# Optimization experiments

Hardware: AMD Instinct MI355X
Metric: run time of the kernel (lower is better)

Reference implementation:

```python
import jax, jax.numpy as jnp
import numpy as np
import math

D_MODEL = 1024
N_HEADS = 16
D_HEAD = 64
D_MLP = 4096
SEQ = 2048
BATCH = 1
BLOCK_INDEX = 2
PREV_NODES = (N_HEADS + 1) * BLOCK_INDEX + 1  # 35
ROTARY_DIM = 64
ROTARY_BASE = 10000
IGNORE = -100000.0
LN_EPS = 1e-5


def setup_inputs() -> dict:
    key = jax.random.key(0)
    ks = jax.random.split(key, 20)
    s = 0.02
    return {
        "resid_pre": jax.random.normal(ks[0], (BATCH, SEQ, PREV_NODES, D_MODEL), jnp.float32),
        "W_Q": s * jax.random.normal(ks[1], (N_HEADS, D_MODEL, D_HEAD), jnp.float32),
        "b_Q": jnp.zeros((N_HEADS, D_HEAD), jnp.float32),
        "W_K": s * jax.random.normal(ks[2], (N_HEADS, D_MODEL, D_HEAD), jnp.float32),
        "b_K": jnp.zeros((N_HEADS, D_HEAD), jnp.float32),
        "W_V": s * jax.random.normal(ks[3], (N_HEADS, D_MODEL, D_HEAD), jnp.float32),
        "b_V": jnp.zeros((N_HEADS, D_HEAD), jnp.float32),
        "W_O": s * jax.random.normal(ks[4], (N_HEADS, D_HEAD, D_MODEL), jnp.float32),
        "b_O": jnp.zeros((D_MODEL,), jnp.float32),
        "mask_q_logits": 0.01 * jax.random.normal(ks[5], (PREV_NODES, N_HEADS), jnp.float32),
        "mask_k_logits": 0.01 * jax.random.normal(ks[6], (PREV_NODES, N_HEADS), jnp.float32),
        "mask_v_logits": 0.01 * jax.random.normal(ks[7], (PREV_NODES, N_HEADS), jnp.float32),
        "mask_mlp_logits": 0.01 * jax.random.normal(ks[8], (PREV_NODES + N_HEADS,), jnp.float32),
        "W_in": s * jax.random.normal(ks[9], (D_MODEL, D_MLP), jnp.float32),
        "b_in": jnp.zeros((D_MLP,), jnp.float32),
        "W_out": s * jax.random.normal(ks[10], (D_MLP, D_MODEL), jnp.float32),
        "b_out": jnp.zeros((D_MODEL,), jnp.float32),
    }


def _rotary_sin_cos(seq_len):
    pos = jnp.arange(seq_len, dtype=jnp.float32)
    dim = jnp.arange(ROTARY_DIM // 2, dtype=jnp.float32)
    freq = ROTARY_BASE ** (dim / (ROTARY_DIM / 2))
    freq = jnp.concatenate([freq, freq])  # '(2 d)' repeat (non-adjacent pairs)
    angles = pos[:, None] / freq[None, :]  # [seq, rotary_dim]
    return jnp.sin(angles), jnp.cos(angles)


def _apply_rotary(x, sin, cos):
    # x: [B, S, H, d_head]; rotary_dim == d_head here
    n = ROTARY_DIM // 2
    x_rot = x[..., :ROTARY_DIM]
    flip = jnp.concatenate([-x_rot[..., n:], x_rot[..., :n]], axis=-1)
    rotated = x_rot * cos[None, :, None, :] + flip * sin[None, :, None, :]
    return jnp.concatenate([rotated, x[..., ROTARY_DIM:]], axis=-1)


def _ln_pre(x):
    # LayerNormPre: center + scale over last dim, no learned params
    x = x - jnp.mean(x, axis=-1, keepdims=True)
    scale = jnp.sqrt(jnp.mean(x * x, axis=-1, keepdims=True) + LN_EPS)
    return x / scale


def reference(resid_pre, W_Q, b_Q, W_K, b_K, W_V, b_V, W_O, b_O,
              mask_q_logits, mask_k_logits, mask_v_logits, mask_mlp_logits,
              W_in, b_in, W_out, b_out):
    B, S = resid_pre.shape[0], resid_pre.shape[1]
    # deterministic edge masks
    m_q = jnp.where(mask_q_logits > 0.0, 1.0, 0.0)
    m_k = jnp.where(mask_k_logits > 0.0, 1.0, 0.0)
    m_v = jnp.where(mask_v_logits > 0.0, 1.0, 0.0)
    m_mlp = jnp.where(mask_mlp_logits > 0.0, 1.0, 0.0)

    # per-head masked residual streams: [B, S, n_heads, d_model]
    res_q = jnp.einsum('bpnm,nh->bphm', resid_pre, m_q)
    res_k = jnp.einsum('bpnm,nh->bphm', resid_pre, m_k)
    res_v = jnp.einsum('bpnm,nh->bphm', resid_pre, m_v)

    nq = _ln_pre(res_q)
    nk = _ln_pre(res_k)
    nv = _ln_pre(res_v)

    # attention (per-head projections)
    q = jnp.einsum('bshm,hmd->bshd', nq, W_Q) + b_Q
    k = jnp.einsum('bshm,hmd->bshd', nk, W_K) + b_K
    sin, cos = _rotary_sin_cos(S)
    q = _apply_rotary(q, sin, cos)
    k = _apply_rotary(k, sin, cos)

    scores = jnp.einsum('bqhd,bkhd->bhqk', q, k) / math.sqrt(D_HEAD)
    causal = jnp.triu(jnp.ones((S, S), dtype=bool), k=1)
    scores = jnp.where(causal[None, None], IGNORE, scores)
    pattern = jax.nn.softmax(scores, axis=-1)

    v = jnp.einsum('bshm,hmd->bshd', nv, W_V) + b_V
    z = jnp.einsum('bhqk,bkhd->bqhd', pattern, v)
    # per-head attn output (heads NOT summed): [B, S, n_heads, d_model]
    attn_out = jnp.einsum('bqhd,hdm->bqhm', z, W_O) + b_O / N_HEADS

    # grow residual stream with attention head nodes
    residual = jnp.concatenate([resid_pre, attn_out], axis=2)  # [B,S,prev+H,dm]

    masked_mlp_residual = jnp.einsum('bpnm,n->bpm', residual, m_mlp)
    norm_mid = _ln_pre(masked_mlp_residual)
    mlp_out = jax.nn.gelu(norm_mid @ W_in + b_in, approximate=True) @ W_out + b_out

    out = jnp.concatenate([residual, mlp_out[:, :, None, :]], axis=2)
    return out
```

## Files before the change

kernel.cpp:

```cpp
#include <hip/hip_runtime.h>
#include <stdint.h>


#define SEQ 2048
#define DM 1024
#define NHEADS 16
#define DH 64
#define DMLP 4096
#define PN 35
#define TOTN 51
#define OUTN 52
#define LNEPS 1e-5f
#define L2E 1.44269504088896340736f

typedef __bf16 bf16x8 __attribute__((ext_vector_type(8)));
typedef float f32x4 __attribute__((ext_vector_type(4)));
typedef unsigned short u16x8 __attribute__((ext_vector_type(8)));

static __device__ __forceinline__ unsigned short f2bf(float f) {
    unsigned int u = __builtin_bit_cast(unsigned int, f);
    u += 0x7fffu + ((u >> 16) & 1u);
    return (unsigned short)(u >> 16);
}

static __device__ __forceinline__ float gelu_tanh(float x) {
    float u = 0.7978845608028654f * x * (1.f + 0.044715f * x * x);
    float e = exp2f(u * (2.f * L2E));
    float th = 1.f - 2.f / (e + 1.f);
    return 0.5f * x * (1.f + th);
}

static __device__ __forceinline__ void gload_lds16(const void* g, void* l) {
    __builtin_amdgcn_global_load_lds(
        (const __attribute__((address_space(1))) unsigned int*)g,
        (__attribute__((address_space(3))) unsigned int*)l, 16, 0, 0);
}

static __device__ __forceinline__ int swz_src(int lane) {
    return ((lane & 7) ^ ((lane >> 3) & 7)) * 8;
}
static __device__ __forceinline__ int swz_off(int r, int g) {
    return ((g ^ (r & 7)) * 16);
}

__global__ void prep_all(const float* __restrict__ mq, const float* __restrict__ mk,
                         const float* __restrict__ mv, const float* __restrict__ mmlp,
                         const float* __restrict__ bQ, const float* __restrict__ bK,
                         const float* __restrict__ bV,
                         float* __restrict__ rot, unsigned long long* __restrict__ maskbits,
                         float* __restrict__ mlpmaskf, float* __restrict__ biasQKV,
                         float* __restrict__ colWqkv, float* __restrict__ colWin) {
    int bid = blockIdx.x, tid = threadIdx.x;
    if (bid < 256) {
        int id = bid * 256 + tid;
        int s = id >> 5, j = id & 31;
        float freq = powf(10000.f, (float)j * (1.f / 32.f));
        float ang = (float)s / freq;
        rot[s * 64 + j] = sinf(ang);
        rot[s * 64 + 32 + j] = cosf(ang);
    } else if (bid == 256) {
        if (tid < 48) {
            int ty = tid >> 4, h = tid & 15;
            const float* src = (ty == 0) ? mq : (ty == 1 ? mk : mv);
            unsigned long long bits = 0;
            for (int n = 0; n < PN; ++n)
                if (src[n * NHEADS + h] > 0.f) bits |= 1ull << n;
            maskbits[tid] = bits;
            const float* bsrc = (ty == 0) ? bQ : (ty == 1 ? bK : bV);
            for (int d = 0; d < DH; ++d) biasQKV[tid * 64 + d] = bsrc[h * DH + d];
        }
        if (tid == 48) {
            unsigned long long bits = 0;
            for (int n = 0; n < PN; ++n)
                if (mmlp[n] > 0.f) bits |= 1ull << n;
            maskbits[48] = bits;
        }
        if (tid < 64) mlpmaskf[tid] = (tid < TOTN && mmlp[tid] > 0.f) ? 1.f : 0.f;
    } else if (bid == 257) {
        for (int i = tid; i < 3072; i += 256) colWqkv[i] = 0.f;
    } else {
        int base = (bid - 258) * 2048;
        for (int i = tid; i < 2048; i += 256) colWin[base + i] = 0.f;
    }
}

__global__ void wtrans(const float* __restrict__ in, unsigned short* __restrict__ out,
                       int K, int N, size_t inZ, size_t outZ,
                       float* __restrict__ colsum, size_t colZ) {
    int z = blockIdx.z;
    const float* ib = in + (size_t)z * inZ;
    unsigned short* ob = out + (size_t)z * outZ;
    __shared__ float t[32][33];
    int n0 = blockIdx.x * 32, k0 = blockIdx.y * 32;
    int tx = threadIdx.x & 31, ty = threadIdx.x >> 5;
#pragma unroll
    for (int r = 0; r < 4; ++r) {
        int k = ty + r * 8;
        t[k][tx] = ib[(size_t)(k0 + k) * N + n0 + tx];
    }
    __syncthreads();
#pragma unroll
    for (int r = 0; r < 4; ++r) {
        int n = ty + r * 8;
        ob[(size_t)(n0 + n) * K + k0 + tx] = f2bf(t[tx][n]);
    }
    if (colsum != nullptr && ty == 0) {
        float s = 0.f;
#pragma unroll
        for (int k = 0; k < 32; ++k) s += t[k][tx];
        atomicAdd(&colsum[(size_t)z * colZ + n0 + tx], s);
    }
}

__launch_bounds__(512, 1)
__global__ void k1_masked_norm(const float* __restrict__ resid,
                               const unsigned long long* __restrict__ maskbits,
                               float* __restrict__ outp,
                               unsigned short* __restrict__ nrm,
                               float* __restrict__ stats,
                               float* __restrict__ prevpart) {
    int s = blockIdx.x;
    int tid = threadIdx.x;
    int lane = tid & 63, w = tid >> 6;
    const float2* rp = (const float2*)(resid + (size_t)s * PN * DM);
    float2* outv = (float2*)(outp + (size_t)s * OUTN * DM);
    float2 r[PN];
#pragma unroll
    for (int n = 0; n < PN; ++n) {
        float2 v = rp[n * (DM / 2) + tid];
        r[n] = v;
        outv[n * (DM / 2) + tid] = v;
    }
    __shared__ float wpart[8][48][2];
#pragma unroll 1
    for (int th = 0; th < 48; ++th) {
        unsigned long long bits = maskbits[th];
        float sx = 0.f, sy = 0.f;
#pragma unroll
        for (int n = 0; n < PN; ++n) {
            if ((bits >> n) & 1ull) { sx += r[n].x; sy += r[n].y; }
        }
        unsigned int pk = (unsigned int)f2bf(sx) | ((unsigned int)f2bf(sy) << 16);
        ((unsigned int*)nrm)[((size_t)th * SEQ + s) * (DM / 2) + tid] = pk;
        float p1 = sx + sy, p2 = sx * sx + sy * sy;
#pragma unroll
        for (int d = 1; d < 64; d <<= 1) {
            p1 += __shfl_xor(p1, d);
            p2 += __shfl_xor(p2, d);
        }
        if (lane == 0) { wpart[w][th][0] = p1; wpart[w][th][1] = p2; }
    }
    {
        unsigned long long bits = maskbits[48];
        float px = 0.f, py = 0.f;
#pragma unroll
        for (int n = 0; n < PN; ++n) {
            if ((bits >> n) & 1ull) { px += r[n].x; py += r[n].y; }
        }
        ((float2*)prevpart)[(size_t)s * (DM / 2) + tid] = make_float2(px, py);
    }
    __syncthreads();
    if (tid < 48) {
        float S1 = 0.f, S2 = 0.f;
        for (int ww = 0; ww < 8; ++ww) { S1 += wpart[ww][tid][0]; S2 += wpart[ww][tid][1]; }
        float mean = S1 * (1.f / DM);
        float var = S2 * (1.f / DM) - mean * mean;
        float* st = stats + ((size_t)tid * SEQ + s) * 2;
        st[0] = mean;
        st[1] = rsqrtf(var + LNEPS);
    }
}

__launch_bounds__(256, 4)
__global__ void stats_k(const float* __restrict__ midf, float* __restrict__ stats) {
    int s = blockIdx.x, tid = threadIdx.x;
    int lane = tid & 63, w = tid >> 6;
    float4 v = ((const float4*)midf)[(size_t)s * (DM / 4) + tid];
    float p1 = v.x + v.y + v.z + v.w;
    float p2 = v.x * v.x + v.y * v.y + v.z * v.z + v.w * v.w;
#pragma unroll
    for (int d = 1; d < 64; d <<= 1) { p1 += __shfl_xor(p1, d); p2 += __shfl_xor(p2, d); }
    __shared__ float wp[4][2];
    if (lane == 0) { wp[w][0] = p1; wp[w][1] = p2; }
    __syncthreads();
    if (tid == 0) {
        float S1 = wp[0][0] + wp[1][0] + wp[2][0] + wp[3][0];
        float S2 = wp[0][1] + wp[1][1] + wp[2][1] + wp[3][1];
        float mean = S1 * (1.f / DM);
        float var = S2 * (1.f / DM) - mean * mean;
        stats[s * 2] = mean;
        stats[s * 2 + 1] = rsqrtf(var + LNEPS);
    }
}

template <int MF, int NF, int WGM, int WGN, int EPI>
__launch_bounds__(256, 2)
__global__ void gemm2(const unsigned short* __restrict__ A, size_t aZ, int lda,
                      const unsigned short* __restrict__ Bt, size_t bZ, int ldb,
                      float* __restrict__ Cf, unsigned short* __restrict__ Cb,
                      size_t cZ, int ldc,
                      const float* __restrict__ stats, size_t statsZ,
                      const float* __restrict__ colW, size_t colwZ,
                      const float* __restrict__ bias, size_t biasZ, float biasScale,
                      const float* __restrict__ rot, unsigned short* __restrict__ Vt,
                      int K) {
    constexpr int BM = WGM * 16 * MF;
    constexpr int BN = WGN * 16 * NF;
    constexpr int nA = BM / 32;
    constexpr int nB = BN / 32;
    __shared__ unsigned short As[BM * 64];
    __shared__ unsigned short Bs[BN * 64];
    const int tid = threadIdx.x;
    const int lane = tid & 63;
    const int w = tid >> 6;
    const int wm = w % WGM, wn = w / WGM;
    const int z = blockIdx.z;
    const int m0 = blockIdx.x * BM;
    const int n0 = blockIdx.y * BN;
    const int cl = lane & 15, rq = lane >> 4;

    const unsigned short* Ab = A + (size_t)z * aZ + (size_t)m0 * lda;
    const unsigned short* Bb = Bt + (size_t)z * bZ + (size_t)n0 * ldb;
    const int lrow8 = lane >> 3;
    const int scol = swz_src(lane);

    f32x4 acc[MF][NF];
#pragma unroll
    for (int mf = 0; mf < MF; ++mf)
#pragma unroll
        for (int nf = 0; nf < NF; ++nf) acc[mf][nf] = 0.f;

    for (int k0 = 0; k0 < K; k0 += 64) {
        __syncthreads();
#pragma unroll
        for (int i = 0; i < nA; ++i) {
            int c = w * nA + i;
            int row = c * 8 + lrow8;
            gload_lds16(Ab + (size_t)row * lda + k0 + scol, (char*)As + c * 1024);
        }
#pragma unroll
        for (int i = 0; i < nB; ++i) {
            int c = w * nB + i;
            int row = c * 8 + lrow8;
            gload_lds16(Bb + (size_t)row * ldb + k0 + scol, (char*)Bs + c * 1024);
        }
        __syncthreads();
#pragma unroll
        for (int ks = 0; ks < 2; ++ks) {
            bf16x8 a[MF], b[NF];
#pragma unroll
            for (int mf = 0; mf < MF; ++mf) {
                int ra = (wm * MF + mf) * 16 + cl;
                a[mf] = *(const bf16x8*)((const char*)As + ra * 128 + swz_off(cl, ks * 4 + rq));
            }
#pragma unroll
            for (int nf = 0; nf < NF; ++nf) {
                int rb = (wn * NF + nf) * 16 + cl;
                b[nf] = *(const bf16x8*)((const char*)Bs + rb * 128 + swz_off(cl, ks * 4 + rq));
            }
#pragma unroll
            for (int mf = 0; mf < MF; ++mf)
#pragma unroll
                for (int nf = 0; nf < NF; ++nf)
                    acc[mf][nf] = __builtin_amdgcn_mfma_f32_16x16x32_bf16(a[mf], b[nf], acc[mf][nf], 0, 0, 0);
        }
    }

    if constexpr (EPI == 0) {
        float* Cz = Cf + (size_t)z * cZ;
        const float* bz = bias + (size_t)z * biasZ;
#pragma unroll
        for (int mf = 0; mf < MF; ++mf)
#pragma unroll
            for (int nf = 0; nf < NF; ++nf) {
                int col = n0 + wn * (16 * NF) + nf * 16 + cl;
                float bv = bz[col] * biasScale;
#pragma unroll
                for (int rr = 0; rr < 4; ++rr) {
                    int row = m0 + wm * (16 * MF) + mf * 16 + rq * 4 + rr;
                    Cz[(size_t)row * ldc + col] = acc[mf][nf][rr] + bv;
                }
            }
    } else if constexpr (EPI == 1) {
        const int t = z >> 4;
        const int h = z & 15;
        const float qs = (t == 0) ? 0.125f : 1.f;
        float vals[MF][NF][4];
        float meanv[MF][4], invv[MF][4];
#pragma unroll
        for (int mf = 0; mf < MF; ++mf)
#pragma unroll
            for (int rr = 0; rr < 4; ++rr) {
                int row = m0 + wm * (16 * MF) + mf * 16 + rq * 4 + rr;
                const float* st = stats + ((size_t)z * statsZ + row) * 2;
                meanv[mf][rr] = st[0];
                invv[mf][rr] = st[1];
            }
#pragma unroll
        for (int nf = 0; nf < NF; ++nf) {
            int col = n0 + wn * (16 * NF) + nf * 16 + cl;
            float cw = colW[(size_t)z * colwZ + col];
            float bv = bias[(size_t)z * biasZ + col];
#pragma unroll
            for (int mf = 0; mf < MF; ++mf)
#pragma unroll
                for (int rr = 0; rr < 4; ++rr)
                    vals[mf][nf][rr] = (acc[mf][nf][rr] - meanv[mf][rr] * cw) * invv[mf][rr] + bv;
        }
        if (t < 2) {
#pragma unroll
            for (int nf = 0; nf < NF / 2; ++nf) {
                int j = nf * 16 + cl;
#pragma unroll
                for (int mf = 0; mf < MF; ++mf)
#pragma unroll
                    for (int rr = 0; rr < 4; ++rr) {
                        int row = m0 + wm * (16 * MF) + mf * 16 + rq * 4 + rr;
                        float sn = rot[row * 64 + j];
                        float cs = rot[row * 64 + 32 + j];
                        float lo = vals[mf][nf][rr], hi = vals[mf][nf + 2][rr];
                        vals[mf][nf][rr] = lo * cs - hi * sn;
                        vals[mf][nf + 2][rr] = hi * cs + lo * sn;
                    }
            }
        }
        if (t == 2) {
#pragma unroll
            for (int mf = 0; mf < MF; ++mf)
#pragma unroll
                for (int nf = 0; nf < NF; ++nf) {
                    int col = nf * 16 + cl;
                    int row0 = m0 + wm * (16 * MF) + mf * 16 + rq * 4;
                    ushort4 pk;
                    pk.x = f2bf(vals[mf][nf][0]);
                    pk.y = f2bf(vals[mf][nf][1]);
                    pk.z = f2bf(vals[mf][nf][2]);
                    pk.w = f2bf(vals[mf][nf][3]);
                    *(ushort4*)&Vt[((size_t)h * DH + col) * SEQ + row0] = pk;
                }
        } else {
            unsigned short* Cz = Cb + (size_t)z * cZ;
#pragma unroll
            for (int mf = 0; mf < MF; ++mf)
#pragma unroll
                for (int nf = 0; nf < NF; ++nf) {
                    int col = n0 + wn * (16 * NF) + nf * 16 + cl;
#pragma unroll
                    for (int rr = 0; rr < 4; ++rr) {
                        int row = m0 + wm * (16 * MF) + mf * 16 + rq * 4 + rr;
                        Cz[(size_t)row * ldc + col] = f2bf(vals[mf][nf][rr] * qs);
                    }
                }
        }
    } else {
        unsigned short* Cz = Cb;
#pragma unroll
        for (int mf = 0; mf < MF; ++mf)
#pragma unroll
            for (int rr = 0; rr < 4; ++rr) {
                int row = m0 + wm * (16 * MF) + mf * 16 + rq * 4 + rr;
                const float* st = stats + (size_t)row * 2;
                float mean = st[0], inv = st[1];
#pragma unroll
                for (int nf = 0; nf < NF; ++nf) {
                    int col = n0 + wn * (16 * NF) + nf * 16 + cl;
                    float x = (acc[mf][nf][rr] - mean * colW[col]) * inv + bias[col];
                    Cz[(size_t)row * ldc + col] = f2bf(gelu_tanh(x));
                }
            }
    }
}

__launch_bounds__(256, 2)
__global__ void flash_k(const unsigned short* __restrict__ qkv,
                        const unsigned short* __restrict__ vt,
                        unsigned short* __restrict__ zbuf) {
    const int p = blockIdx.x, h = blockIdx.y;
    const int tid = threadIdx.x, lane = tid & 63, w = tid >> 6;
    const int cl = lane & 15, rq = lane >> 4;
    const int lrow8 = lane >> 3;
    const int scol = swz_src(lane);
    const unsigned short* qb = qkv + ((size_t)h * SEQ) * DH;
    const unsigned short* kb = qkv + ((size_t)(16 + h) * SEQ) * DH;
    const unsigned short* vtb = vt + (size_t)h * DH * SEQ;

    __shared__ unsigned short Ks[64 * 64];
    __shared__ unsigned short Vs[64 * 64];
    __shared__ unsigned short Ps[64][72];

#pragma unroll 1
    for (int half = 0; half < 2; ++half) {
        const int qi = half ? (31 - p) : p;
        const int q0 = qi * 64;

        bf16x8 aq[2];
        {
            int qrow = q0 + w * 16 + cl;
            const unsigned short* qp = qb + (size_t)qrow * DH + rq * 8;
            aq[0] = *(const bf16x8*)(qp);
            aq[1] = *(const bf16x8*)(qp + 32);
        }
        float m_run[4] = {-3e38f, -3e38f, -3e38f, -3e38f};
        float l_run[4] = {0.f, 0.f, 0.f, 0.f};
        f32x4 accz[4];
#pragma unroll
        for (int nf = 0; nf < 4; ++nf) accz[nf] = 0.f;

#pragma unroll 1
        for (int j = 0; j <= qi; ++j) {
            __syncthreads();
#pragma unroll
            for (int i = 0; i < 2; ++i) {
                int c = w * 2 + i;
                int row = c * 8 + lrow8;
                gload_lds16(kb + (size_t)(j * 64 + row) * DH + scol, (char*)Ks + c * 1024);
                gload_lds16(vtb + (size_t)row * SEQ + j * 64 + scol, (char*)Vs + c * 1024);
            }
            __syncthreads();

            f32x4 sfr[4];
#pragma unroll
            for (int nf = 0; nf < 4; ++nf) sfr[nf] = 0.f;
#pragma unroll
            for (int df = 0; df < 2; ++df)
#pragma unroll
                for (int nf = 0; nf < 4; ++nf) {
                    int rb = nf * 16 + cl;
                    bf16x8 b = *(const bf16x8*)((const char*)Ks + rb * 128 + swz_off(cl, df * 4 + rq));
                    sfr[nf] = __builtin_amdgcn_mfma_f32_16x16x32_bf16(aq[df], b, sfr[nf], 0, 0, 0);
                }
            if (j == qi) {
#pragma unroll
                for (int nf = 0; nf < 4; ++nf)
#pragma unroll
                    for (int rr = 0; rr < 4; ++rr) {
                        int qg = q0 + w * 16 + rq * 4 + rr;
                        int kg = j * 64 + nf * 16 + cl;
                        if (kg > qg) sfr[nf][rr] = -1e5f;
                    }
            }
            float mnew[4], corr[4], psum[4];
#pragma unroll
            for (int rr = 0; rr < 4; ++rr) {
                float t0 = fmaxf(fmaxf(sfr[0][rr], sfr[1][rr]), fmaxf(sfr[2][rr], sfr[3][rr]));
                t0 = fmaxf(t0, __shfl_xor(t0, 1));
                t0 = fmaxf(t0, __shfl_xor(t0, 2));
                t0 = fmaxf(t0, __shfl_xor(t0, 4));
                t0 = fmaxf(t0, __shfl_xor(t0, 8));
                mnew[rr] = fmaxf(m_run[rr], t0);
                corr[rr] = exp2f((m_run[rr] - mnew[rr]) * L2E);
                psum[rr] = 0.f;
            }
#pragma unroll
            for (int nf = 0; nf < 4; ++nf)
#pragma unroll
                for (int rr = 0; rr < 4; ++rr) {
                    float pv = exp2f((sfr[nf][rr] - mnew[rr]) * L2E);
                    sfr[nf][rr] = pv;
                    psum[rr] += pv;
                }
#pragma unroll
            for (int rr = 0; rr < 4; ++rr) {
                float ps = psum[rr];
                ps += __shfl_xor(ps, 1);
                ps += __shfl_xor(ps, 2);
                ps += __shfl_xor(ps, 4);
                ps += __shfl_xor(ps, 8);
                l_run[rr] = l_run[rr] * corr[rr] + ps;
                m_run[rr] = mnew[rr];
            }
#pragma unroll
            for (int nf = 0; nf < 4; ++nf)
#pragma unroll
                for (int rr = 0; rr < 4; ++rr) accz[nf][rr] *= corr[rr];

#pragma unroll
            for (int nf = 0; nf < 4; ++nf)
#pragma unroll
                for (int rr = 0; rr < 4; ++rr)
                    Ps[w * 16 + rq * 4 + rr][nf * 16 + cl] = f2bf(sfr[nf][rr]);
#pragma unroll
            for (int ks = 0; ks < 2; ++ks) {
                bf16x8 ap = *(const bf16x8*)&Ps[w * 16 + cl][ks * 32 + rq * 8];
#pragma unroll
                for (int nf = 0; nf < 4; ++nf) {
                    int rb = nf * 16 + cl;
                    bf16x8 bv = *(const bf16x8*)((const char*)Vs + rb * 128 + swz_off(cl, ks * 4 + rq));
                    accz[nf] = __builtin_amdgcn_mfma_f32_16x16x32_bf16(ap, bv, accz[nf], 0, 0, 0);
                }
            }
        }
#pragma unroll
        for (int nf = 0; nf < 4; ++nf)
#pragma unroll
            for (int rr = 0; rr < 4; ++rr) {
                int qg = q0 + w * 16 + rq * 4 + rr;
                zbuf[((size_t)h * SEQ + qg) * DH + nf * 16 + cl] = f2bf(accz[nf][rr] / l_run[rr]);
            }
        __syncthreads();
    }
}

__launch_bounds__(256, 2)
__global__ void attn_fused(const unsigned short* __restrict__ zbuf,
                           const unsigned short* __restrict__ WtO,
                           const float* __restrict__ bO,
                           const float* __restrict__ mlpmaskf,
                           const float* __restrict__ prevpart,
                           float* __restrict__ outp,
                           unsigned short* __restrict__ midb,
                           float* __restrict__ midf) {
    __shared__ unsigned short As[64 * 64];
    __shared__ unsigned short Bs[128 * 64];
    const int tid = threadIdx.x;
    const int lane = tid & 63;
    const int w = tid >> 6;
    const int cl = lane & 15, rq = lane >> 4;
    const int lrow8 = lane >> 3;
    const int scol = swz_src(lane);
    const int m0 = blockIdx.x * 64;
    const int n0 = blockIdx.y * 128;

    f32x4 macc[4][2];
#pragma unroll
    for (int mf = 0; mf < 4; ++mf)
#pragma unroll
        for (int nf = 0; nf < 2; ++nf)
#pragma unroll
            for (int rr = 0; rr < 4; ++rr) {
                int row = m0 + mf * 16 + rq * 4 + rr;
                int col = n0 + w * 32 + nf * 16 + cl;
                macc[mf][nf][rr] = prevpart[(size_t)row * DM + col];
            }

#pragma unroll 1
    for (int h = 0; h < NHEADS; ++h) {
        __syncthreads();
#pragma unroll
        for (int i = 0; i < 2; ++i) {
            int c = w * 2 + i;
            int row = c * 8 + lrow8;
            gload_lds16(zbuf + ((size_t)h * SEQ + m0 + row) * DH + scol, (char*)As + c * 1024);
        }
#pragma unroll
        for (int i = 0; i < 4; ++i) {
            int c = w * 4 + i;
            int row = c * 8 + lrow8;
            gload_lds16(WtO + ((size_t)h * DM + n0 + row) * DH + scol, (char*)Bs + c * 1024);
        }
        __syncthreads();
        f32x4 acc[4][2];
#pragma unroll
        for (int mf = 0; mf < 4; ++mf)
#pragma unroll
            for (int nf = 0; nf < 2; ++nf) acc[mf][nf] = 0.f;
#pragma unroll
        for (int ks = 0; ks < 2; ++ks) {
            bf16x8 a[4], b[2];
#pragma unroll
            for (int mf = 0; mf < 4; ++mf) {
                int ra = mf * 16 + cl;
                a[mf] = *(const bf16x8*)((const char*)As + ra * 128 + swz_off(cl, ks * 4 + rq));
            }
#pragma unroll
            for (int nf = 0; nf < 2; ++nf) {
                int rb = w * 32 + nf * 16 + cl;
                b[nf] = *(const bf16x8*)((const char*)Bs + rb * 128 + swz_off(cl, ks * 4 + rq));
            }
#pragma unroll
            for (int mf = 0; mf < 4; ++mf)
#pragma unroll
                for (int nf = 0; nf < 2; ++nf)
                    acc[mf][nf] = __builtin_amdgcn_mfma_f32_16x16x32_bf16(a[mf], b[nf], acc[mf][nf], 0, 0, 0);
        }
        float mh = mlpmaskf[PN + h];
#pragma unroll
        for (int nf = 0; nf < 2; ++nf) {
            int col = n0 + w * 32 + nf * 16 + cl;
            float bv = bO[col] * (1.f / 16.f);
#pragma unroll
            for (int mf = 0; mf < 4; ++mf)
#pragma unroll
                for (int rr = 0; rr < 4; ++rr) {
                    int row = m0 + mf * 16 + rq * 4 + rr;
                    float v = acc[mf][nf][rr] + bv;
                    outp[(size_t)row * (OUTN * DM) + (PN + h) * DM + col] = v;
                    macc[mf][nf][rr] += mh * v;
                }
        }
    }
#pragma unroll
    for (int mf = 0; mf < 4; ++mf)
#pragma unroll
        for (int nf = 0; nf < 2; ++nf) {
            int col = n0 + w * 32 + nf * 16 + cl;
#pragma unroll
            for (int rr = 0; rr < 4; ++rr) {
                int row = m0 + mf * 16 + rq * 4 + rr;
                float v = macc[mf][nf][rr];
                midf[(size_t)row * DM + col] = v;
                midb[(size_t)row * DM + col] = f2bf(v);
            }
        }
}

extern "C" void kernel_launch(void* const* d_in, const int* in_sizes, int n_in,
                              void* d_out, int out_size, void* d_ws, size_t ws_size,
                              hipStream_t stream) {
    const float* resid = (const float*)d_in[0];
    const float* W_Q = (const float*)d_in[1];
    const float* b_Q = (const float*)d_in[2];
    const float* W_K = (const float*)d_in[3];
    const float* b_K = (const float*)d_in[4];
    const float* W_V = (const float*)d_in[5];
    const float* b_V = (const float*)d_in[6];
    const float* W_O = (const float*)d_in[7];
    const float* b_O = (const float*)d_in[8];
    const float* mql = (const float*)d_in[9];
    const float* mkl = (const float*)d_in[10];
    const float* mvl = (const float*)d_in[11];
    const float* mml = (const float*)d_in[12];
    const float* W_in = (const float*)d_in[13];
    const float* b_in = (const float*)d_in[14];
    const float* W_out = (const float*)d_in[15];
    const float* b_out = (const float*)d_in[16];
    float* out = (float*)d_out;
    (void)in_sizes; (void)n_in; (void)out_size; (void)ws_size;

    char* ws = (char*)d_ws;
    size_t off = 0;
    auto carve = [&](size_t bytes) -> void* {
        void* p = ws + off;
        off += (bytes + 255) & ~(size_t)255;
        return p;
    };
    unsigned short* nrm = (unsigned short*)carve((size_t)48 * SEQ * DM * 2);
    float* statsQ = (float*)carve((size_t)48 * SEQ * 2 * 4);
    unsigned short* qkv = (unsigned short*)carve((size_t)48 * SEQ * DH * 2);
    unsigned short* vtb = (unsigned short*)carve((size_t)NHEADS * DH * SEQ * 2);
    unsigned short* zbuf = (unsigned short*)carve((size_t)NHEADS * SEQ * DH * 2);
    unsigned short* midb = (unsigned short*)carve((size_t)SEQ * DM * 2);
    float* midf = (float*)carve((size_t)SEQ * DM * 4);
    float* statsM = (float*)carve((size_t)SEQ * 2 * 4);
    unsigned short* act = (unsigned short*)carve((size_t)SEQ * DMLP * 2);
    float* rot = (float*)carve((size_t)SEQ * 64 * 4);
    float* colWqkv = (float*)carve((size_t)48 * 64 * 4);
    float* colWin = (float*)carve((size_t)DMLP * 4);
    float* mlpmaskf = (float*)carve((size_t)64 * 4);
    float* biasQKV = (float*)carve((size_t)48 * 64 * 4);
    unsigned long long* maskbits = (unsigned long long*)carve((size_t)64 * 8);
    float* prevpart = (float*)carve((size_t)SEQ * DM * 4);
    unsigned short* WtQKV = (unsigned short*)carve((size_t)48 * DH * DM * 2);
    unsigned short* WtO = (unsigned short*)carve((size_t)16 * DM * DH * 2);
    unsigned short* WtIn = (unsigned short*)carve((size_t)DMLP * DM * 2);
    unsigned short* WtOut = (unsigned short*)carve((size_t)DM * DMLP * 2);

    prep_all<<<260, 256, 0, stream>>>(mql, mkl, mvl, mml, b_Q, b_K, b_V,
                                      rot, maskbits, mlpmaskf, biasQKV, colWqkv, colWin);

    wtrans<<<dim3(2, 32, 16), 256, 0, stream>>>(W_Q, WtQKV, DM, DH, (size_t)DM * DH, (size_t)DH * DM, colWqkv, 64);
    wtrans<<<dim3(2, 32, 16), 256, 0, stream>>>(W_K, WtQKV + (size_t)16 * DH * DM, DM, DH, (size_t)DM * DH, (size_t)DH * DM, colWqkv + 1024, 64);
    wtrans<<<dim3(2, 32, 16), 256, 0, stream>>>(W_V, WtQKV + (size_t)32 * DH * DM, DM, DH, (size_t)DM * DH, (size_t)DH * DM, colWqkv + 2048, 64);
    wtrans<<<dim3(32, 2, 16), 256, 0, stream>>>(W_O, WtO, DH, DM, (size_t)DH * DM, (size_t)DM * DH, nullptr, 0);
    wtrans<<<dim3(128, 32, 1), 256, 0, stream>>>(W_in, WtIn, DM, DMLP, 0, 0, colWin, 0);
    wtrans<<<dim3(32, 128, 1), 256, 0, stream>>>(W_out, WtOut, DMLP, DM, 0, 0, nullptr, 0);

    k1_masked_norm<<<SEQ, 512, 0, stream>>>(resid, maskbits, out, nrm, statsQ, prevpart);

    gemm2<2, 4, 4, 1, 1><<<dim3(16, 1, 48), 256, 0, stream>>>(
        nrm, (size_t)SEQ * DM, DM,
        WtQKV, (size_t)DH * DM, DM,
        nullptr, qkv, (size_t)SEQ * DH, DH,
        statsQ, SEQ,
        colWqkv, 64,
        biasQKV, 64, 1.f,
        rot, vtb, DM);

    flash_k<<<dim3(16, 16), 256, 0, stream>>>(qkv, vtb, zbuf);

    attn_fused<<<dim3(32, 8), 256, 0, stream>>>(zbuf, WtO, b_O, mlpmaskf, prevpart, out, midb, midf);

    stats_k<<<SEQ, 256, 0, stream>>>(midf, statsM);

    gemm2<4, 4, 2, 2, 2><<<dim3(16, 32, 1), 256, 0, stream>>>(
        midb, 0, DM,
        WtIn, 0, DM,
        nullptr, act, 0, DMLP,
        statsM, 0,
        colWin, 0,
        b_in, 0, 1.f,
        nullptr, nullptr, DM);

    gemm2<2, 4, 2, 2, 0><<<dim3(32, 8, 1), 256, 0, stream>>>(
        act, 0, DMLP,
        WtOut, 0, DMLP,
        out + 51 * DM, nullptr, 0, OUTN * DM,
        nullptr, 0, nullptr, 0,
        b_out, 0, 1.f,
        nullptr, nullptr, DMLP);
}
```

Measured before the change: 578.5 us.

## Fuse MLP LayerNorm stats into attn output, merge transposes, restructure masked-norm

Folds the separate stats_k pass into attn_fused: per-row sum and sum-of-squares are reduced with shuffles and accumulated with atomics into a buffer zeroed by prep_all. This removes the fp32 midf write and read. The MLP-in gemm now derives mean and inverse std from those raw sums. The six weight-transpose launches are merged into one kernel. k1_masked_norm now streams over nodes, accumulating 48 masked sums in registers via per-node bitmasks, and packs bf16 with v_cvt_pk_bf16_f32. Risks: atomic contention, register pressure or spills from 96 accumulators under the tighter launch bound, and a slightly different reduction order.

```diff
diff --git a/kernel.cpp b/kernel.cpp
--- a/kernel.cpp
+++ b/kernel.cpp
@@ -23,6 +23,12 @@
     return (unsigned short)(u >> 16);
 }
 
+static __device__ __forceinline__ unsigned int cvt_pk_bf16(float lo, float hi) {
+    unsigned int pk;
+    asm("v_cvt_pk_bf16_f32 %0, %1, %2" : "=v"(pk) : "v"(lo), "v"(hi));
+    return pk;
+}
+
 static __device__ __forceinline__ float gelu_tanh(float x) {
     float u = 0.7978845608028654f * x * (1.f + 0.044715f * x * x);
     float e = exp2f(u * (2.f * L2E));
@@ -47,9 +53,10 @@
                          const float* __restrict__ mv, const float* __restrict__ mmlp,
                          const float* __restrict__ bQ, const float* __restrict__ bK,
                          const float* __restrict__ bV,
-                         float* __restrict__ rot, unsigned long long* __restrict__ maskbits,
+                         float* __restrict__ rot, unsigned long long* __restrict__ nodebits,
                          float* __restrict__ mlpmaskf, float* __restrict__ biasQKV,
-                         float* __restrict__ colWqkv, float* __restrict__ colWin) {
+                         float* __restrict__ colWqkv, float* __restrict__ colWin,
+                         float* __restrict__ statsM2) {
     int bid = blockIdx.x, tid = threadIdx.x;
     if (bid < 256) {
         int id = bid * 256 + tid;
@@ -59,62 +66,100 @@
         rot[s * 64 + j] = sinf(ang);
         rot[s * 64 + 32 + j] = cosf(ang);
     } else if (bid == 256) {
-        if (tid < 48) {
-            int ty = tid >> 4, h = tid & 15;
-            const float* src = (ty == 0) ? mq : (ty == 1 ? mk : mv);
+        if (tid < PN) {
+            int n = tid;
             unsigned long long bits = 0;
-            for (int n = 0; n < PN; ++n)
-                if (src[n * NHEADS + h] > 0.f) bits |= 1ull << n;
-            maskbits[tid] = bits;
+            for (int h = 0; h < NHEADS; ++h) {
+                if (mq[n * NHEADS + h] > 0.f) bits |= 1ull << (0 * 16 + h);
+                if (mk[n * NHEADS + h] > 0.f) bits |= 1ull << (1 * 16 + h);
+                if (mv[n * NHEADS + h] > 0.f) bits |= 1ull << (2 * 16 + h);
+            }
+            if (mmlp[n] > 0.f) bits |= 1ull << 48;
+            nodebits[n] = bits;
+        }
+        if (tid >= 64 && tid < 112) {
+            int t = tid - 64;
+            int ty = t >> 4, h = t & 15;
             const float* bsrc = (ty == 0) ? bQ : (ty == 1 ? bK : bV);
-            for (int d = 0; d < DH; ++d) biasQKV[tid * 64 + d] = bsrc[h * DH + d];
-        }
-        if (tid == 48) {
-            unsigned long long bits = 0;
-            for (int n = 0; n < PN; ++n)
-                if (mmlp[n] > 0.f) bits |= 1ull << n;
-            maskbits[48] = bits;
-        }
-        if (tid < 64) mlpmaskf[tid] = (tid < TOTN && mmlp[tid] > 0.f) ? 1.f : 0.f;
+            for (int d = 0; d < DH; ++d) biasQKV[t * 64 + d] = bsrc[h * DH + d];
+        }
+        if (tid >= 112 && tid < 176) {
+            int i = tid - 112;
+            mlpmaskf[i] = (i < TOTN && mmlp[i] > 0.f) ? 1.f : 0.f;
+        }
     } else if (bid == 257) {
         for (int i = tid; i < 3072; i += 256) colWqkv[i] = 0.f;
-    } else {
+    } else if (bid == 258 || bid == 259) {
         int base = (bid - 258) * 2048;
         for (int i = tid; i < 2048; i += 256) colWin[base + i] = 0.f;
-    }
-}
-
-__global__ void wtrans(const float* __restrict__ in, unsigned short* __restrict__ out,
-                       int K, int N, size_t inZ, size_t outZ,
-                       float* __restrict__ colsum, size_t colZ) {
-    int z = blockIdx.z;
-    const float* ib = in + (size_t)z * inZ;
-    unsigned short* ob = out + (size_t)z * outZ;
+    } else {
+        for (int i = tid; i < SEQ * 2; i += 256) statsM2[i] = 0.f;
+    }
+}
+
+__global__ void wtrans_all(const float* __restrict__ WQ, const float* __restrict__ WK,
+                           const float* __restrict__ WV, const float* __restrict__ WO,
+                           const float* __restrict__ Win, const float* __restrict__ Wout,
+                           unsigned short* __restrict__ WtQKV, unsigned short* __restrict__ WtO,
+                           unsigned short* __restrict__ WtIn, unsigned short* __restrict__ WtOut,
+                           float* __restrict__ colWqkv, float* __restrict__ colWin) {
+    int bid = blockIdx.x;
+    const float* src; unsigned short* dst;
+    int K, N, n0, k0;
+    float* cs = nullptr;
+    if (bid < 3072) {
+        int ty = bid >> 10;
+        int b = bid & 1023;
+        int z = b >> 6, r = b & 63;
+        int zeff = ty * 16 + z;
+        src = ((ty == 0) ? WQ : (ty == 1 ? WK : WV)) + (size_t)z * DM * DH;
+        dst = WtQKV + (size_t)zeff * DH * DM;
+        K = DM; N = DH;
+        n0 = (r & 1) * 32; k0 = (r >> 1) * 32;
+        cs = colWqkv + zeff * 64;
+    } else if (bid < 4096) {
+        int b = bid - 3072;
+        int z = b >> 6, r = b & 63;
+        src = WO + (size_t)z * DH * DM;
+        dst = WtO + (size_t)z * DM * DH;
+        K = DH; N = DM;
+        n0 = (r & 31) * 32; k0 = (r >> 5) * 32;
+    } else if (bid < 8192) {
+        int b = bid - 4096;
+        src = Win; dst = WtIn;
+        K = DM; N = DMLP;
+        n0 = (b & 127) * 32; k0 = (b >> 7) * 32;
+        cs = colWin;
+    } else {
+        int b = bid - 8192;
+        src = Wout; dst = WtOut;
+        K = DMLP; N = DM;
+        n0 = (b & 31) * 32; k0 = (b >> 5) * 32;
+    }
     __shared__ float t[32][33];
-    int n0 = blockIdx.x * 32, k0 = blockIdx.y * 32;
-    int tx = threadIdx.x & 31, ty = threadIdx.x >> 5;
+    int tx = threadIdx.x & 31, ty2 = threadIdx.x >> 5;
 #pragma unroll
     for (int r = 0; r < 4; ++r) {
-        int k = ty + r * 8;
-        t[k][tx] = ib[(size_t)(k0 + k) * N + n0 + tx];
+        int k = ty2 + r * 8;
+        t[k][tx] = src[(size_t)(k0 + k) * N + n0 + tx];
     }
     __syncthreads();
 #pragma unroll
     for (int r = 0; r < 4; ++r) {
-        int n = ty + r * 8;
-        ob[(size_t)(n0 + n) * K + k0 + tx] = f2bf(t[tx][n]);
-    }
-    if (colsum != nullptr && ty == 0) {
+        int n = ty2 + r * 8;
+        dst[(size_t)(n0 + n) * K + k0 + tx] = f2bf(t[tx][n]);
+    }
+    if (cs != nullptr && ty2 == 0) {
         float s = 0.f;
 #pragma unroll
         for (int k = 0; k < 32; ++k) s += t[k][tx];
-        atomicAdd(&colsum[(size_t)z * colZ + n0 + tx], s);
-    }
-}
-
-__launch_bounds__(512, 1)
+        atomicAdd(&cs[n0 + tx], s);
+    }
+}
+
+__launch_bounds__(512, 4)
 __global__ void k1_masked_norm(const float* __restrict__ resid,
-                               const unsigned long long* __restrict__ maskbits,
+                               const unsigned long long* __restrict__ nodebits,
                                float* __restrict__ outp,
                                unsigned short* __restrict__ nrm,
                                float* __restrict__ stats,
@@ -124,40 +169,38 @@
     int lane = tid & 63, w = tid >> 6;
     const float2* rp = (const float2*)(resid + (size_t)s * PN * DM);
     float2* outv = (float2*)(outp + (size_t)s * OUTN * DM);
-    float2 r[PN];
-#pragma unroll
+    float ax[48], ay[48];
+#pragma unroll
+    for (int t = 0; t < 48; ++t) { ax[t] = 0.f; ay[t] = 0.f; }
+    float px = 0.f, py = 0.f;
+#pragma unroll 1
     for (int n = 0; n < PN; ++n) {
+        unsigned long long nb = nodebits[n];
         float2 v = rp[n * (DM / 2) + tid];
-        r[n] = v;
         outv[n * (DM / 2) + tid] = v;
-    }
+#pragma unroll
+        for (int t = 0; t < 48; ++t) {
+            float f = ((nb >> t) & 1ull) ? 1.0f : 0.0f;
+            ax[t] += f * v.x;
+            ay[t] += f * v.y;
+        }
+        float f48 = ((nb >> 48) & 1ull) ? 1.0f : 0.0f;
+        px += f48 * v.x;
+        py += f48 * v.y;
+    }
+    ((float2*)prevpart)[(size_t)s * (DM / 2) + tid] = make_float2(px, py);
     __shared__ float wpart[8][48][2];
-#pragma unroll 1
-    for (int th = 0; th < 48; ++th) {
-        unsigned long long bits = maskbits[th];
-        float sx = 0.f, sy = 0.f;
-#pragma unroll
-        for (int n = 0; n < PN; ++n) {
-            if ((bits >> n) & 1ull) { sx += r[n].x; sy += r[n].y; }
-        }
-        unsigned int pk = (unsigned int)f2bf(sx) | ((unsigned int)f2bf(sy) << 16);
-        ((unsigned int*)nrm)[((size_t)th * SEQ + s) * (DM / 2) + tid] = pk;
-        float p1 = sx + sy, p2 = sx * sx + sy * sy;
+#pragma unroll
+    for (int t = 0; t < 48; ++t) {
+        ((unsigned int*)nrm)[((size_t)t * SEQ + s) * (DM / 2) + tid] = cvt_pk_bf16(ax[t], ay[t]);
+        float p1 = ax[t] + ay[t];
+        float p2 = ax[t] * ax[t] + ay[t] * ay[t];
 #pragma unroll
         for (int d = 1; d < 64; d <<= 1) {
             p1 += __shfl_xor(p1, d);
             p2 += __shfl_xor(p2, d);
         }
-        if (lane == 0) { wpart[w][th][0] = p1; wpart[w][th][1] = p2; }
-    }
-    {
-        unsigned long long bits = maskbits[48];
-        float px = 0.f, py = 0.f;
-#pragma unroll
-        for (int n = 0; n < PN; ++n) {
-            if ((bits >> n) & 1ull) { px += r[n].x; py += r[n].y; }
-        }
-        ((float2*)prevpart)[(size_t)s * (DM / 2) + tid] = make_float2(px, py);
+        if (lane == 0) { wpart[w][t][0] = p1; wpart[w][t][1] = p2; }
     }
     __syncthreads();
     if (tid < 48) {
@@ -168,28 +211,6 @@
         float* st = stats + ((size_t)tid * SEQ + s) * 2;
         st[0] = mean;
         st[1] = rsqrtf(var + LNEPS);
-    }
-}
-
-__launch_bounds__(256, 4)
-__global__ void stats_k(const float* __restrict__ midf, float* __restrict__ stats) {
-    int s = blockIdx.x, tid = threadIdx.x;
-    int lane = tid & 63, w = tid >> 6;
-    float4 v = ((const float4*)midf)[(size_t)s * (DM / 4) + tid];
-    float p1 = v.x + v.y + v.z + v.w;
-    float p2 = v.x * v.x + v.y * v.y + v.z * v.z + v.w * v.w;
-#pragma unroll
-    for (int d = 1; d < 64; d <<= 1) { p1 += __shfl_xor(p1, d); p2 += __shfl_xor(p2, d); }
-    __shared__ float wp[4][2];
-    if (lane == 0) { wp[w][0] = p1; wp[w][1] = p2; }
-    __syncthreads();
-    if (tid == 0) {
-        float S1 = wp[0][0] + wp[1][0] + wp[2][0] + wp[3][0];
-        float S2 = wp[0][1] + wp[1][1] + wp[2][1] + wp[3][1];
-        float mean = S1 * (1.f / DM);
-        float var = S2 * (1.f / DM) - mean * mean;
-        stats[s * 2] = mean;
-        stats[s * 2 + 1] = rsqrtf(var + LNEPS);
     }
 }
 
@@ -359,8 +380,10 @@
 #pragma unroll
             for (int rr = 0; rr < 4; ++rr) {
                 int row = m0 + wm * (16 * MF) + mf * 16 + rq * 4 + rr;
-                const float* st = stats + (size_t)row * 2;
-                float mean = st[0], inv = st[1];
+                float S1 = stats[(size_t)row * 2];
+                float S2 = stats[(size_t)row * 2 + 1];
+                float mean = S1 * (1.f / DM);
+                float inv = rsqrtf(S2 * (1.f / DM) - mean * mean + LNEPS);
 #pragma unroll
                 for (int nf = 0; nf < NF; ++nf) {
                     int col = n0 + wn * (16 * NF) + nf * 16 + cl;
@@ -509,7 +532,7 @@
                            const float* __restrict__ prevpart,
                            float* __restrict__ outp,
                            unsigned short* __restrict__ midb,
-                           float* __restrict__ midf) {
+                           float* __restrict__ statsM2) {
     __shared__ unsigned short As[64 * 64];
     __shared__ unsigned short Bs[128 * 64];
     const int tid = threadIdx.x;
@@ -592,14 +615,22 @@
 #pragma unroll
     for (int mf = 0; mf < 4; ++mf)
 #pragma unroll
-        for (int nf = 0; nf < 2; ++nf) {
-            int col = n0 + w * 32 + nf * 16 + cl;
-#pragma unroll
-            for (int rr = 0; rr < 4; ++rr) {
-                int row = m0 + mf * 16 + rq * 4 + rr;
-                float v = macc[mf][nf][rr];
-                midf[(size_t)row * DM + col] = v;
-                midb[(size_t)row * DM + col] = f2bf(v);
+        for (int rr = 0; rr < 4; ++rr) {
+            float v0 = macc[mf][0][rr], v1 = macc[mf][1][rr];
+            int row = m0 + mf * 16 + rq * 4 + rr;
+            int col0 = n0 + w * 32 + cl;
+            midb[(size_t)row * DM + col0] = f2bf(v0);
+            midb[(size_t)row * DM + col0 + 16] = f2bf(v1);
+            float s1 = v0 + v1;
+            float s2 = v0 * v0 + v1 * v1;
+#pragma unroll
+            for (int d = 1; d < 16; d <<= 1) {
+                s1 += __shfl_xor(s1, d);
+                s2 += __shfl_xor(s2, d);
+            }
+            if (cl == 0) {
+                atomicAdd(&statsM2[row * 2], s1);
+                atomicAdd(&statsM2[row * 2 + 1], s2);
             }
         }
 }
@@ -640,32 +671,28 @@
     unsigned short* vtb = (unsigned short*)carve((size_t)NHEADS * DH * SEQ * 2);
     unsigned short* zbuf = (unsigned short*)carve((size_t)NHEADS * SEQ * DH * 2);
     unsigned short* midb = (unsigned short*)carve((size_t)SEQ * DM * 2);
-    float* midf = (float*)carve((size_t)SEQ * DM * 4);
-    float* statsM = (float*)carve((size_t)SEQ * 2 * 4);
+    float* statsM2 = (float*)carve((size_t)SEQ * 2 * 4);
     unsigned short* act = (unsigned short*)carve((size_t)SEQ * DMLP * 2);
     float* rot = (float*)carve((size_t)SEQ * 64 * 4);
     float* colWqkv = (float*)carve((size_t)48 * 64 * 4);
     float* colWin = (float*)carve((size_t)DMLP * 4);
     float* mlpmaskf = (float*)carve((size_t)64 * 4);
     float* biasQKV = (float*)carve((size_t)48 * 64 * 4);
-    unsigned long long* maskbits = (unsigned long long*)carve((size_t)64 * 8);
+    unsigned long long* nodebits = (unsigned long long*)carve((size_t)64 * 8);
     float* prevpart = (float*)carve((size_t)SEQ * DM * 4);
     unsigned short* WtQKV = (unsigned short*)carve((size_t)48 * DH * DM * 2);
     unsigned short* WtO = (unsigned short*)carve((size_t)16 * DM * DH * 2);
     unsigned short* WtIn = (unsigned short*)carve((size_t)DMLP * DM * 2);
     unsigned short* WtOut = (unsigned short*)carve((size_t)DM * DMLP * 2);
 
-    prep_all<<<260, 256, 0, stream>>>(mql, mkl, mvl, mml, b_Q, b_K, b_V,
-                                      rot, maskbits, mlpmaskf, biasQKV, colWqkv, colWin);
-
-    wtrans<<<dim3(2, 32, 16), 256, 0, stream>>>(W_Q, WtQKV, DM, DH, (size_t)DM * DH, (size_t)DH * DM, colWqkv, 64);
-    wtrans<<<dim3(2, 32, 16), 256, 0, stream>>>(W_K, WtQKV + (size_t)16 * DH * DM, DM, DH, (size_t)DM * DH, (size_t)DH * DM, colWqkv + 1024, 64);
-    wtrans<<<dim3(2, 32, 16), 256, 0, stream>>>(W_V, WtQKV + (size_t)32 * DH * DM, DM, DH, (size_t)DM * DH, (size_t)DH * DM, colWqkv + 2048, 64);
-    wtrans<<<dim3(32, 2, 16), 256, 0, stream>>>(W_O, WtO, DH, DM, (size_t)DH * DM, (size_t)DM * DH, nullptr, 0);
-    wtrans<<<dim3(128, 32, 1), 256, 0, stream>>>(W_in, WtIn, DM, DMLP, 0, 0, colWin, 0);
-    wtrans<<<dim3(32, 128, 1), 256, 0, stream>>>(W_out, WtOut, DMLP, DM, 0, 0, nullptr, 0);
-
-    k1_masked_norm<<<SEQ, 512, 0, stream>>>(resid, maskbits, out, nrm, statsQ, prevpart);
+    prep_all<<<261, 256, 0, stream>>>(mql, mkl, mvl, mml, b_Q, b_K, b_V,
+                                      rot, nodebits, mlpmaskf, biasQKV,
+                                      colWqkv, colWin, statsM2);
+
+    wtrans_all<<<12288, 256, 0, stream>>>(W_Q, W_K, W_V, W_O, W_in, W_out,
+                                          WtQKV, WtO, WtIn, WtOut, colWqkv, colWin);
+
+    k1_masked_norm<<<SEQ, 512, 0, stream>>>(resid, nodebits, out, nrm, statsQ, prevpart);
 
     gemm2<2, 4, 4, 1, 1><<<dim3(16, 1, 48), 256, 0, stream>>>(
         nrm, (size_t)SEQ * DM, DM,
@@ -678,15 +705,14 @@
 
     flash_k<<<dim3(16, 16), 256, 0, stream>>>(qkv, vtb, zbuf);
 
-    attn_fused<<<dim3(32, 8), 256, 0, stream>>>(zbuf, WtO, b_O, mlpmaskf, prevpart, out, midb, midf);
-
-    stats_k<<<SEQ, 256, 0, stream>>>(midf, statsM);
+    attn_fused<<<dim3(32, 8), 256, 0, stream>>>(zbuf, WtO, b_O, mlpmaskf, prevpart,
+                                                out, midb, statsM2);
 
     gemm2<4, 4, 2, 2, 2><<<dim3(16, 32, 1), 256, 0, stream>>>(
         midb, 0, DM,
         WtIn, 0, DM,
         nullptr, act, 0, DMLP,
-        statsM, 0,
+        statsM2, 0,
         colWin, 0,
         b_in, 0, 1.f,
         nullptr, nullptr, DM);
```

Measured after the change: 785.9 us. 35.8% more time.
